# Kernel optimization log

Measured on AMD Instinct MI355X. Metric: run time of the kernel, lower is better.

Reference implementation:

```python
import math
import jax, jax.numpy as jnp
import numpy as np

# ---- module hyperparameters (from init_kwargs) ----
N_DELTA, N_THETA, N_GAMMA = 32, 64, 256
N_TOTAL = N_DELTA + N_THETA + N_GAMMA  # 352
N_DIMS = 1024
BATCH = 4096
N_STEPS = 32
DT = 0.01
COUPLING = 2.0
PAC = 0.3
EPS = 1e-6
TWO_PI = 2.0 * math.pi


def setup_inputs() -> dict:
    key = jax.random.key(0)
    k0, k1, k2 = jax.random.split(key, 3)
    x = jax.random.normal(k0, (BATCH, N_DIMS), dtype=jnp.float32)
    # xavier_uniform with gain=0.5 for Linear(n_dims, n_total, bias=False)
    bound = 0.5 * math.sqrt(6.0 / (N_DIMS + N_TOTAL))
    W_phase = jax.random.uniform(k1, (N_TOTAL, N_DIMS), jnp.float32, -bound, bound)
    W_amp = jax.random.uniform(k2, (N_TOTAL, N_DIMS), jnp.float32, -bound, bound)
    # natural angular frequencies per band: delta ~2Hz, theta ~6Hz, gamma ~40Hz
    omega = jnp.concatenate([
        jnp.full((N_DELTA,), TWO_PI * 2.0, jnp.float32),
        jnp.full((N_THETA,), TWO_PI * 6.0, jnp.float32),
        jnp.full((N_GAMMA,), TWO_PI * 40.0, jnp.float32),
    ])
    # block-diagonal intra-band Kuramoto coupling, K_ij = coupling_strength / n_band
    Kn = np.zeros((N_TOTAL, N_TOTAL), dtype=np.float32)
    o = 0
    for nb in (N_DELTA, N_THETA, N_GAMMA):
        Kn[o:o + nb, o:o + nb] = COUPLING / nb
        o += nb
    K = jnp.asarray(Kn)
    return {"x": x, "W_phase": W_phase, "W_amp": W_amp, "omega": omega, "K": K}


def reference(x, W_phase, W_amp, omega, K):
    # learned projections -> initial phase in [0, 2pi), amplitude clamped >= eps
    phase0 = (x @ W_phase.T) % TWO_PI                      # (B, n_total)
    amp0 = jnp.maximum(jnp.abs(x @ W_amp.T), EPS)          # (B, n_total)

    def step(carry, _):
        phase, amp = carry
        s, c = jnp.sin(phase), jnp.cos(phase)
        # sum_j K_ij sin(phi_j - phi_i) = cos(phi_i)*(K@sin)_i - sin(phi_i)*(K@cos)_i
        coup = c * (s @ K.T) - s * (c @ K.T)
        phase_n = (phase + DT * (omega + coup)) % TWO_PI
        d = phase_n[:, :N_DELTA]
        t = phase_n[:, N_DELTA:N_DELTA + N_THETA]
        mean_d = jnp.arctan2(jnp.sin(d).mean(-1), jnp.cos(d).mean(-1))  # (B,)
        mean_t = jnp.arctan2(jnp.sin(t).mean(-1), jnp.cos(t).mean(-1))  # (B,)
        B = phase.shape[0]
        mod = jnp.concatenate([
            jnp.zeros((B, N_DELTA), phase.dtype),
            jnp.broadcast_to((PAC * jnp.cos(mean_d))[:, None], (B, N_THETA)),
            jnp.broadcast_to((PAC * jnp.cos(mean_t))[:, None], (B, N_GAMMA)),
        ], axis=-1)
        amp_n = jnp.maximum(amp * (1.0 + DT * mod), EPS)
        return (phase_n, amp_n), None

    (final_phase, final_amp), _ = jax.lax.scan(step, (phase0, amp0), None, length=N_STEPS)
    return final_amp
```

## Files before the change

### kernel.cpp

```cpp
#include <hip/hip_runtime.h>

typedef float  f32x4 __attribute__((ext_vector_type(4)));
typedef short  s16x8 __attribute__((ext_vector_type(8)));
typedef _Float16 h2 __attribute__((ext_vector_type(2)));
typedef unsigned short u16;
typedef u16 u16x4 __attribute__((ext_vector_type(4)));

#define N_DIMS 1024
#define N_OSC  352
#define N_PH   96
#define BATCH  4096
#define EPSV   1e-6f
#define INV2PI 0.15915494309189535f

__device__ __forceinline__ u16 f2bf(float f){
  unsigned u = __builtin_bit_cast(unsigned, f);
  u += 0x7FFFu + ((u >> 16) & 1u);
  return (u16)(u >> 16);
}
__device__ __forceinline__ float bf2f(unsigned h){
  return __builtin_bit_cast(float, h << 16);
}

#define NX4 1048576
#define NWP4 24576
#define NWA4 90112
#define NCONV (NX4 + NWP4 + NWA4)

__global__ __launch_bounds__(256) void convert_k(const f32x4* __restrict__ x,
    const f32x4* __restrict__ wp, const f32x4* __restrict__ wa,
    u16x4* __restrict__ xb, u16x4* __restrict__ wb){
  int i = blockIdx.x * 256 + threadIdx.x;
  if (i >= NCONV) return;
  f32x4 v; u16x4* dst;
  if (i < NX4) { v = x[i]; dst = xb + i; }
  else {
    int j = i - NX4;
    v = (j < NWP4) ? wp[j] : wa[j - NWP4];
    dst = wb + j;
  }
  u16x4 r;
  r[0]=f2bf(v[0]); r[1]=f2bf(v[1]); r[2]=f2bf(v[2]); r[3]=f2bf(v[3]);
  *dst = r;
}

__device__ __forceinline__ void gload16(const u16* g, u16* l){
  __builtin_amdgcn_global_load_lds(
      (const __attribute__((address_space(1))) unsigned int*)(g),
      (__attribute__((address_space(3))) unsigned int*)(l), 16, 0, 0);
}

__global__ __launch_bounds__(256) void gemm_k(const u16* __restrict__ xb,
    const u16* __restrict__ wb, u16* __restrict__ phase0, float* __restrict__ amp0){
  __shared__ u16 lds[2][6144];
  const int tid = threadIdx.x;
  const int l   = tid & 63;
  const int w   = tid >> 6;

  const int bid = blockIdx.x;
  const int xcd = bid & 7;
  const int r   = bid >> 3;
  const int mt  = xcd * 8 + r / 14;
  const int nt  = r % 14;
  const int m0  = mt * 64;
  const int n0  = nt * 32;

  const int sr8  = l >> 3;
  const int scol = (((l & 7) ^ sr8) * 8);
  const u16* ga = xb + (size_t)(m0 + w*16 + sr8) * N_DIMS + scol;
  const u16* gb = wb + (size_t)(n0 + w*8  + sr8) * N_DIMS + scol;

  #define STAGE(b, kt) { \
    gload16(ga + (kt)*64,            &lds[b][w*1024]); \
    gload16(ga + (kt)*64 + 8*N_DIMS, &lds[b][w*1024 + 512]); \
    gload16(gb + (kt)*64,            &lds[b][4096 + w*512]); }

  const int rl = l & 15;
  const int q0 = l >> 4;
  const int sx = l & 7;
  const int wr = w >> 1, wc = w & 1;

  f32x4 acc[2] = {};
  STAGE(0, 0)
  __syncthreads();

  for (int kt = 0; kt < 16; kt++){
    const int cb = kt & 1;
    if (kt < 15) STAGE(cb^1, kt+1)
    s16x8 a[2][2], b[2];
    #pragma unroll
    for (int mi = 0; mi < 2; mi++)
    #pragma unroll
    for (int ks = 0; ks < 2; ks++){
      int off = (wr*32 + mi*16 + rl)*64 + (((ks*4 + q0) ^ sx) * 8);
      a[mi][ks] = *(const s16x8*)&lds[cb][off];
    }
    #pragma unroll
    for (int ks = 0; ks < 2; ks++){
      int off = 4096 + (wc*16 + rl)*64 + (((ks*4 + q0) ^ sx) * 8);
      b[ks] = *(const s16x8*)&lds[cb][off];
    }
    #pragma unroll
    for (int ks = 0; ks < 2; ks++)
    #pragma unroll
    for (int mi = 0; mi < 2; mi++)
      acc[mi] = __builtin_amdgcn_mfma_f32_16x16x32_bf16(a[mi][ks], b[ks], acc[mi], 0,0,0);
    __syncthreads();
  }
  #undef STAGE

  const int n = n0 + wc*16 + rl;
  const bool isph = (n < N_PH);
  #pragma unroll
  for (int mi = 0; mi < 2; mi++)
  #pragma unroll
  for (int rg = 0; rg < 4; rg++){
    const int m = m0 + wr*32 + mi*16 + q0*4 + rg;
    float v = acc[mi][rg];
    if (isph){ float t = v * INV2PI; t -= floorf(t); phase0[(size_t)m*N_PH + n] = f2bf(t); }
    else     { amp0[(size_t)m*N_OSC + (n - N_PH)] = fmaxf(fabsf(v), EPSV); }
  }
}

__device__ __forceinline__ int ibc(h2 v){ return __builtin_bit_cast(int, v); }
__device__ __forceinline__ h2  hbc(int v){ return __builtin_bit_cast(h2, v); }

__device__ __forceinline__ h2 rowsum16(h2 x){
  int v = ibc(x);
  v = ibc(hbc(v) + hbc(__builtin_amdgcn_mov_dpp(v, 0x121, 0xF, 0xF, true)));
  v = ibc(hbc(v) + hbc(__builtin_amdgcn_mov_dpp(v, 0x122, 0xF, 0xF, true)));
  v = ibc(hbc(v) + hbc(__builtin_amdgcn_mov_dpp(v, 0x124, 0xF, 0xF, true)));
  v = ibc(hbc(v) + hbc(__builtin_amdgcn_mov_dpp(v, 0x128, 0xF, 0xF, true)));
  return hbc(v);
}

__device__ __forceinline__ void updp(h2& s, h2& c, h2 cA, h2 sA, h2 GS, h2 GC){
  h2 e  = c*GS - s*GC;
  h2 s1 = s*cA + c*sA;
  h2 c1 = c*cA - s*sA;
  s = s1 + c1*e;
  c = c1 - s1*e;
}

__device__ __forceinline__ h2 splat2(_Float16 v){ h2 r; r[0]=v; r[1]=v; return r; }

__global__ __launch_bounds__(256) void iter_k(const u16* __restrict__ phase0,
                                              float* __restrict__ amp){
  const int tid = threadIdx.x;
  const int l   = tid & 63;
  const int g   = l & 15;
  const int row = blockIdx.x*16 + (tid>>6)*4 + (l>>4);
  const size_t rb  = (size_t)row * N_OSC;
  const size_t rbp = (size_t)row * N_PH;

  const h2 cAd = splat2((_Float16)0.99211470f), sAd = splat2((_Float16)0.12533323f);
  const h2 cAt = splat2((_Float16)0.92977649f), sAt = splat2((_Float16)0.36812455f);
  const h2 kd = splat2((_Float16)6.25e-4f);
  const h2 kt = splat2((_Float16)3.125e-4f);

  h2 sD, cD, sT[2], cT[2];
  {
    const u16* pr = phase0 + rbp;
    unsigned dw = *(const unsigned*)(pr + 2*g);
    uint2 tw    = *(const uint2*)(pr + 32 + 4*g);
    #define SC2(dS, dC, i, p0, p1) { \
      dS[i][0] = (_Float16)__builtin_amdgcn_sinf(p0); \
      dS[i][1] = (_Float16)__builtin_amdgcn_sinf(p1); \
      dC[i][0] = (_Float16)__builtin_amdgcn_cosf(p0); \
      dC[i][1] = (_Float16)__builtin_amdgcn_cosf(p1); }
    {
      float d0 = bf2f(dw & 0xFFFFu), d1 = bf2f(dw >> 16);
      sD[0] = (_Float16)__builtin_amdgcn_sinf(d0);
      sD[1] = (_Float16)__builtin_amdgcn_sinf(d1);
      cD[0] = (_Float16)__builtin_amdgcn_cosf(d0);
      cD[1] = (_Float16)__builtin_amdgcn_cosf(d1);
    }
    SC2(sT, cT, 0, bf2f(tw.x & 0xFFFFu), bf2f(tw.x >> 16))
    SC2(sT, cT, 1, bf2f(tw.y & 0xFFFFu), bf2f(tw.y >> 16))
    #undef SC2
  }

  h2 PD, PT;
  #define REDUCE { \
    h2 pd; pd[0] = sD[0]+sD[1]; pd[1] = cD[0]+cD[1]; \
    h2 ts = sT[0]+sT[1], tc = cT[0]+cT[1]; \
    h2 pt; pt[0] = ts[0]+ts[1]; pt[1] = tc[0]+tc[1]; \
    PD = rowsum16(pd); PT = rowsum16(pt); }

  REDUCE

  float Pth = 1.f, Pga = 1.f, mPth = 1.f, mPga = 1.f;
  for (int t = 0; t < 32; t++){
    h2 gd = PD * kd, gt = PT * kt;
    h2 GSd = splat2(gd[0]), GCd = splat2(gd[1]);
    h2 GSt = splat2(gt[0]), GCt = splat2(gt[1]);
    updp(sD, cD, cAd, sAd, GSd, GCd);
    updp(sT[0], cT[0], cAt, sAt, GSt, GCt);
    updp(sT[1], cT[1], cAt, sAt, GSt, GCt);
    REDUCE
    float Sd = (float)PD[0], Cd = (float)PD[1];
    float St = (float)PT[0], Ct = (float)PT[1];
    float ft = 1.f + 0.003f * Cd * __builtin_amdgcn_rsqf(Cd*Cd + Sd*Sd);
    float fg = 1.f + 0.003f * Ct * __builtin_amdgcn_rsqf(Ct*Ct + St*St);
    Pth *= ft; mPth = fminf(mPth, Pth);
    Pga *= fg; mPga = fminf(mPga, Pga);
  }
  #undef REDUCE

  const float cth = EPSV * Pth / mPth;
  const float cga = EPSV * Pga / mPga;
  {
    float4 a = *(const float4*)(amp + rb + 32 + 4*g);
    a.x = fmaxf(a.x*Pth, cth); a.y = fmaxf(a.y*Pth, cth);
    a.z = fmaxf(a.z*Pth, cth); a.w = fmaxf(a.w*Pth, cth);
    *(float4*)(amp + rb + 32 + 4*g) = a;
  }
  #pragma unroll
  for (int i = 0; i < 4; i++){
    float4 a = *(const float4*)(amp + rb + 96 + 16*g + 4*i);
    a.x = fmaxf(a.x*Pga, cga); a.y = fmaxf(a.y*Pga, cga);
    a.z = fmaxf(a.z*Pga, cga); a.w = fmaxf(a.w*Pga, cga);
    *(float4*)(amp + rb + 96 + 16*g + 4*i) = a;
  }
}

extern "C" void kernel_launch(void* const* d_in, const int* in_sizes, int n_in,
                              void* d_out, int out_size, void* d_ws, size_t ws_size,
                              hipStream_t stream){
  const float* x  = (const float*)d_in[0];
  const float* wp = (const float*)d_in[1];
  const float* wa = (const float*)d_in[2];
  float* out = (float*)d_out;
  char* ws = (char*)d_ws;
  u16* xb  = (u16*)(ws);
  u16* wb  = (u16*)(ws + 8388608);
  u16* phase0 = (u16*)(ws + 9306112);

  convert_k<<<4544, 256, 0, stream>>>((const f32x4*)x, (const f32x4*)wp, (const f32x4*)wa,
                                      (u16x4*)xb, (u16x4*)wb);
  gemm_k<<<896, 256, 0, stream>>>(xb, wb, phase0, out);
  iter_k<<<256, 256, 0, stream>>>(phase0, out);
}
```

Baseline: 31.22 us.

## Fuse phase GEMM and oscillator iteration into prep kernel, apply amp factors in GEMM epilogue

```diff
diff --git a/kernel.cpp b/kernel.cpp
--- a/kernel.cpp
+++ b/kernel.cpp
@@ -18,113 +18,27 @@
   u += 0x7FFFu + ((u >> 16) & 1u);
   return (u16)(u >> 16);
 }
-__device__ __forceinline__ float bf2f(unsigned h){
-  return __builtin_bit_cast(float, h << 16);
-}
-
-#define NX4 1048576
-#define NWP4 24576
-#define NWA4 90112
-#define NCONV (NX4 + NWP4 + NWA4)
-
-__global__ __launch_bounds__(256) void convert_k(const f32x4* __restrict__ x,
-    const f32x4* __restrict__ wp, const f32x4* __restrict__ wa,
-    u16x4* __restrict__ xb, u16x4* __restrict__ wb){
-  int i = blockIdx.x * 256 + threadIdx.x;
-  if (i >= NCONV) return;
-  f32x4 v; u16x4* dst;
-  if (i < NX4) { v = x[i]; dst = xb + i; }
-  else {
-    int j = i - NX4;
-    v = (j < NWP4) ? wp[j] : wa[j - NWP4];
-    dst = wb + j;
-  }
-  u16x4 r;
-  r[0]=f2bf(v[0]); r[1]=f2bf(v[1]); r[2]=f2bf(v[2]); r[3]=f2bf(v[3]);
-  *dst = r;
-}
-
+__device__ __forceinline__ unsigned pkbf(float a, float b){
+  unsigned r; asm("v_cvt_pk_bf16_f32 %0, %1, %2" : "=v"(r) : "v"(a), "v"(b)); return r;
+}
+__device__ __forceinline__ s16x8 mk8(f32x4 a, f32x4 b){
+  uint4 u; u.x = pkbf(a[0],a[1]); u.y = pkbf(a[2],a[3]);
+  u.z = pkbf(b[0],b[1]); u.w = pkbf(b[2],b[3]);
+  return __builtin_bit_cast(s16x8, u);
+}
 __device__ __forceinline__ void gload16(const u16* g, u16* l){
   __builtin_amdgcn_global_load_lds(
       (const __attribute__((address_space(1))) unsigned int*)(g),
       (__attribute__((address_space(3))) unsigned int*)(l), 16, 0, 0);
 }
-
-__global__ __launch_bounds__(256) void gemm_k(const u16* __restrict__ xb,
-    const u16* __restrict__ wb, u16* __restrict__ phase0, float* __restrict__ amp0){
-  __shared__ u16 lds[2][6144];
-  const int tid = threadIdx.x;
-  const int l   = tid & 63;
-  const int w   = tid >> 6;
-
-  const int bid = blockIdx.x;
-  const int xcd = bid & 7;
-  const int r   = bid >> 3;
-  const int mt  = xcd * 8 + r / 14;
-  const int nt  = r % 14;
-  const int m0  = mt * 64;
-  const int n0  = nt * 32;
-
-  const int sr8  = l >> 3;
-  const int scol = (((l & 7) ^ sr8) * 8);
-  const u16* ga = xb + (size_t)(m0 + w*16 + sr8) * N_DIMS + scol;
-  const u16* gb = wb + (size_t)(n0 + w*8  + sr8) * N_DIMS + scol;
-
-  #define STAGE(b, kt) { \
-    gload16(ga + (kt)*64,            &lds[b][w*1024]); \
-    gload16(ga + (kt)*64 + 8*N_DIMS, &lds[b][w*1024 + 512]); \
-    gload16(gb + (kt)*64,            &lds[b][4096 + w*512]); }
-
-  const int rl = l & 15;
-  const int q0 = l >> 4;
-  const int sx = l & 7;
-  const int wr = w >> 1, wc = w & 1;
-
-  f32x4 acc[2] = {};
-  STAGE(0, 0)
-  __syncthreads();
-
-  for (int kt = 0; kt < 16; kt++){
-    const int cb = kt & 1;
-    if (kt < 15) STAGE(cb^1, kt+1)
-    s16x8 a[2][2], b[2];
-    #pragma unroll
-    for (int mi = 0; mi < 2; mi++)
-    #pragma unroll
-    for (int ks = 0; ks < 2; ks++){
-      int off = (wr*32 + mi*16 + rl)*64 + (((ks*4 + q0) ^ sx) * 8);
-      a[mi][ks] = *(const s16x8*)&lds[cb][off];
-    }
-    #pragma unroll
-    for (int ks = 0; ks < 2; ks++){
-      int off = 4096 + (wc*16 + rl)*64 + (((ks*4 + q0) ^ sx) * 8);
-      b[ks] = *(const s16x8*)&lds[cb][off];
-    }
-    #pragma unroll
-    for (int ks = 0; ks < 2; ks++)
-    #pragma unroll
-    for (int mi = 0; mi < 2; mi++)
-      acc[mi] = __builtin_amdgcn_mfma_f32_16x16x32_bf16(a[mi][ks], b[ks], acc[mi], 0,0,0);
-    __syncthreads();
-  }
-  #undef STAGE
-
-  const int n = n0 + wc*16 + rl;
-  const bool isph = (n < N_PH);
-  #pragma unroll
-  for (int mi = 0; mi < 2; mi++)
-  #pragma unroll
-  for (int rg = 0; rg < 4; rg++){
-    const int m = m0 + wr*32 + mi*16 + q0*4 + rg;
-    float v = acc[mi][rg];
-    if (isph){ float t = v * INV2PI; t -= floorf(t); phase0[(size_t)m*N_PH + n] = f2bf(t); }
-    else     { amp0[(size_t)m*N_OSC + (n - N_PH)] = fmaxf(fabsf(v), EPSV); }
-  }
+__device__ __forceinline__ void gload16f(const float* g, float* l){
+  __builtin_amdgcn_global_load_lds(
+      (const __attribute__((address_space(1))) unsigned int*)(g),
+      (__attribute__((address_space(3))) unsigned int*)(l), 16, 0, 0);
 }
 
 __device__ __forceinline__ int ibc(h2 v){ return __builtin_bit_cast(int, v); }
 __device__ __forceinline__ h2  hbc(int v){ return __builtin_bit_cast(h2, v); }
-
 __device__ __forceinline__ h2 rowsum16(h2 x){
   int v = ibc(x);
   v = ibc(hbc(v) + hbc(__builtin_amdgcn_mov_dpp(v, 0x121, 0xF, 0xF, true)));
@@ -133,7 +47,6 @@
   v = ibc(hbc(v) + hbc(__builtin_amdgcn_mov_dpp(v, 0x128, 0xF, 0xF, true)));
   return hbc(v);
 }
-
 __device__ __forceinline__ void updp(h2& s, h2& c, h2 cA, h2 sA, h2 GS, h2 GC){
   h2 e  = c*GS - s*GC;
   h2 s1 = s*cA + c*sA;
@@ -141,57 +54,127 @@
   s = s1 + c1*e;
   c = c1 - s1*e;
 }
-
 __device__ __forceinline__ h2 splat2(_Float16 v){ h2 r; r[0]=v; r[1]=v; return r; }
 
-__global__ __launch_bounds__(256) void iter_k(const u16* __restrict__ phase0,
-                                              float* __restrict__ amp){
+#define NX4 1048576
+#define NWA4 90112
+
+__global__ __launch_bounds__(256) void prep_k(const float* __restrict__ x,
+    const float* __restrict__ wp, const float* __restrict__ wa,
+    u16x4* __restrict__ xb, u16x4* __restrict__ wb, float* __restrict__ factors){
+  __shared__ float ldsf[14336];
   const int tid = threadIdx.x;
-  const int l   = tid & 63;
-  const int g   = l & 15;
-  const int row = blockIdx.x*16 + (tid>>6)*4 + (l>>4);
-  const size_t rb  = (size_t)row * N_OSC;
-  const size_t rbp = (size_t)row * N_PH;
+  const int bid = blockIdx.x;
+
+  if (bid >= 256){
+    int i = (bid - 256)*256 + tid;
+    f32x4 v; u16x4* dst;
+    if (i < NX4) { v = ((const f32x4*)x)[i]; dst = xb + i; }
+    else { int j = i - NX4; v = ((const f32x4*)wa)[j]; dst = wb + j; }
+    u16x4 r;
+    r[0]=f2bf(v[0]); r[1]=f2bf(v[1]); r[2]=f2bf(v[2]); r[3]=f2bf(v[3]);
+    *dst = r;
+    return;
+  }
+
+  const int m0 = bid * 16;
+  const int l  = tid & 63;
+  const int w  = tid >> 6;
+  const int rl = l & 15;
+  const int q0 = l >> 4;
+
+  const int tr = tid >> 4;
+  const int ts = tid & 15;
+  const int ss = ts ^ tr;
+  const float* gx = x  + (size_t)(m0 + tr) * N_DIMS + ss*4;
+  const float* gw = wp + (size_t)tr * N_DIMS + ss*4;
+
+  #define PSTAGE(b, kt) { \
+    gload16f(gx + (kt)*64, &ldsf[(b)*7168 + tid*4]); \
+    _Pragma("unroll") \
+    for (int i = 0; i < 6; i++) \
+      gload16f(gw + (size_t)i*16384 + (kt)*64, &ldsf[(b)*7168 + 1024 + i*1024 + tid*4]); }
+
+  f32x4 acc[3] = {};
+  PSTAGE(0, 0)
+  __syncthreads();
+
+  const int s0 = (w & 1)*8 + q0*2;
+  const int gb = (w >> 1) * 3;
+
+  for (int kt = 0; kt < 16; kt++){
+    const int cb = kt & 1;
+    if (kt < 15) PSTAGE(cb^1, kt+1)
+    f32x4 a0 = *(const f32x4*)&ldsf[cb*7168 + rl*64 + ((s0     ^ rl) * 4)];
+    f32x4 a1 = *(const f32x4*)&ldsf[cb*7168 + rl*64 + (((s0+1) ^ rl) * 4)];
+    s16x8 af = mk8(a0, a1);
+    #pragma unroll
+    for (int ng = 0; ng < 3; ng++){
+      const int rowb = (gb + ng)*16 + rl;
+      f32x4 b0 = *(const f32x4*)&ldsf[cb*7168 + 1024 + rowb*64 + ((s0     ^ rl) * 4)];
+      f32x4 b1 = *(const f32x4*)&ldsf[cb*7168 + 1024 + rowb*64 + (((s0+1) ^ rl) * 4)];
+      acc[ng] = __builtin_amdgcn_mfma_f32_16x16x32_bf16(af, mk8(b0, b1), acc[ng], 0,0,0);
+    }
+    __syncthreads();
+  }
+  #undef PSTAGE
+
+  #pragma unroll
+  for (int ng = 0; ng < 3; ng++)
+    *(f32x4*)&ldsf[w*768 + ng*256 + l*4] = acc[ng];
+  __syncthreads();
+
+  if (!(w & 1)){
+    #pragma unroll
+    for (int ng = 0; ng < 3; ng++){
+      const int G = gb + ng;
+      f32x4 s = *(const f32x4*)&ldsf[ w   *768 + ng*256 + l*4]
+              + *(const f32x4*)&ldsf[(w+1)*768 + ng*256 + l*4];
+      #pragma unroll
+      for (int rg = 0; rg < 4; rg++){
+        const int row = q0*4 + rg;
+        float t = s[rg] * INV2PI; t -= floorf(t);
+        ldsf[4096 + row*96 + G*16 + rl] = t;
+      }
+    }
+  }
+  __syncthreads();
+
+  const int row16 = w*4 + q0;
+  const int g = rl;
+  const float* ph = &ldsf[4096 + row16*96];
 
   const h2 cAd = splat2((_Float16)0.99211470f), sAd = splat2((_Float16)0.12533323f);
   const h2 cAt = splat2((_Float16)0.92977649f), sAt = splat2((_Float16)0.36812455f);
   const h2 kd = splat2((_Float16)6.25e-4f);
-  const h2 kt = splat2((_Float16)3.125e-4f);
+  const h2 kt2 = splat2((_Float16)3.125e-4f);
 
   h2 sD, cD, sT[2], cT[2];
   {
-    const u16* pr = phase0 + rbp;
-    unsigned dw = *(const unsigned*)(pr + 2*g);
-    uint2 tw    = *(const uint2*)(pr + 32 + 4*g);
-    #define SC2(dS, dC, i, p0, p1) { \
-      dS[i][0] = (_Float16)__builtin_amdgcn_sinf(p0); \
-      dS[i][1] = (_Float16)__builtin_amdgcn_sinf(p1); \
-      dC[i][0] = (_Float16)__builtin_amdgcn_cosf(p0); \
-      dC[i][1] = (_Float16)__builtin_amdgcn_cosf(p1); }
-    {
-      float d0 = bf2f(dw & 0xFFFFu), d1 = bf2f(dw >> 16);
-      sD[0] = (_Float16)__builtin_amdgcn_sinf(d0);
-      sD[1] = (_Float16)__builtin_amdgcn_sinf(d1);
-      cD[0] = (_Float16)__builtin_amdgcn_cosf(d0);
-      cD[1] = (_Float16)__builtin_amdgcn_cosf(d1);
-    }
-    SC2(sT, cT, 0, bf2f(tw.x & 0xFFFFu), bf2f(tw.x >> 16))
-    SC2(sT, cT, 1, bf2f(tw.y & 0xFFFFu), bf2f(tw.y >> 16))
-    #undef SC2
+    float d0 = ph[2*g], d1 = ph[2*g+1];
+    float4 tw = *(const float4*)&ph[32 + 4*g];
+    sD[0] = (_Float16)__builtin_amdgcn_sinf(d0);
+    sD[1] = (_Float16)__builtin_amdgcn_sinf(d1);
+    cD[0] = (_Float16)__builtin_amdgcn_cosf(d0);
+    cD[1] = (_Float16)__builtin_amdgcn_cosf(d1);
+    sT[0][0] = (_Float16)__builtin_amdgcn_sinf(tw.x); sT[0][1] = (_Float16)__builtin_amdgcn_sinf(tw.y);
+    cT[0][0] = (_Float16)__builtin_amdgcn_cosf(tw.x); cT[0][1] = (_Float16)__builtin_amdgcn_cosf(tw.y);
+    sT[1][0] = (_Float16)__builtin_amdgcn_sinf(tw.z); sT[1][1] = (_Float16)__builtin_amdgcn_sinf(tw.w);
+    cT[1][0] = (_Float16)__builtin_amdgcn_cosf(tw.z); cT[1][1] = (_Float16)__builtin_amdgcn_cosf(tw.w);
   }
 
   h2 PD, PT;
   #define REDUCE { \
     h2 pd; pd[0] = sD[0]+sD[1]; pd[1] = cD[0]+cD[1]; \
-    h2 ts = sT[0]+sT[1], tc = cT[0]+cT[1]; \
-    h2 pt; pt[0] = ts[0]+ts[1]; pt[1] = tc[0]+tc[1]; \
+    h2 ts_ = sT[0]+sT[1], tc_ = cT[0]+cT[1]; \
+    h2 pt; pt[0] = ts_[0]+ts_[1]; pt[1] = tc_[0]+tc_[1]; \
     PD = rowsum16(pd); PT = rowsum16(pt); }
 
   REDUCE
 
   float Pth = 1.f, Pga = 1.f, mPth = 1.f, mPga = 1.f;
   for (int t = 0; t < 32; t++){
-    h2 gd = PD * kd, gt = PT * kt;
+    h2 gd = PD * kd, gt = PT * kt2;
     h2 GSd = splat2(gd[0]), GCd = splat2(gd[1]);
     h2 GSt = splat2(gt[0]), GCt = splat2(gt[1]);
     updp(sD, cD, cAd, sAd, GSd, GCd);
@@ -207,20 +190,86 @@
   }
   #undef REDUCE
 
-  const float cth = EPSV * Pth / mPth;
-  const float cga = EPSV * Pga / mPga;
-  {
-    float4 a = *(const float4*)(amp + rb + 32 + 4*g);
-    a.x = fmaxf(a.x*Pth, cth); a.y = fmaxf(a.y*Pth, cth);
-    a.z = fmaxf(a.z*Pth, cth); a.w = fmaxf(a.w*Pth, cth);
-    *(float4*)(amp + rb + 32 + 4*g) = a;
-  }
+  if (rl == 0){
+    float4 f; f.x = Pth; f.y = EPSV * Pth / mPth; f.z = Pga; f.w = EPSV * Pga / mPga;
+    *(float4*)(factors + (size_t)(m0 + row16)*4) = f;
+  }
+}
+
+__global__ __launch_bounds__(256) void gemm_k(const u16* __restrict__ xb,
+    const u16* __restrict__ wb, const float* __restrict__ factors,
+    float* __restrict__ out){
+  __shared__ u16 lds[2][6144];
+  const int tid = threadIdx.x;
+  const int l   = tid & 63;
+  const int w   = tid >> 6;
+
+  const int bid = blockIdx.x;
+  const int xcd = bid & 7;
+  const int r   = bid >> 3;
+  const int mt  = xcd * 8 + r / 11;
+  const int nt  = r % 11;
+  const int m0  = mt * 64;
+  const int n0  = nt * 32;
+
+  const int sr8  = l >> 3;
+  const int scol = (((l & 7) ^ sr8) * 8);
+  const u16* gA0 = xb + (size_t)(m0 + w*16 + sr8) * N_DIMS + scol;
+  const u16* gB0 = wb + (size_t)(n0 + w*8  + sr8) * N_DIMS + scol;
+
+  #define STAGE(b, kt) { \
+    gload16(gA0 + (kt)*64,            &lds[b][w*1024]); \
+    gload16(gA0 + (kt)*64 + 8*N_DIMS, &lds[b][w*1024 + 512]); \
+    gload16(gB0 + (kt)*64,            &lds[b][4096 + w*512]); }
+
+  const int rl = l & 15;
+  const int q0 = l >> 4;
+  const int sx = l & 7;
+  const int wr = w >> 1, wc = w & 1;
+
+  f32x4 acc[2] = {};
+  STAGE(0, 0)
+  __syncthreads();
+
+  for (int kt = 0; kt < 16; kt++){
+    const int cb = kt & 1;
+    if (kt < 15) STAGE(cb^1, kt+1)
+    s16x8 a[2][2], b[2];
+    #pragma unroll
+    for (int mi = 0; mi < 2; mi++)
+    #pragma unroll
+    for (int ks = 0; ks < 2; ks++){
+      int off = (wr*32 + mi*16 + rl)*64 + (((ks*4 + q0) ^ sx) * 8);
+      a[mi][ks] = *(const s16x8*)&lds[cb][off];
+    }
+    #pragma unroll
+    for (int ks = 0; ks < 2; ks++){
+      int off = 4096 + (wc*16 + rl)*64 + (((ks*4 + q0) ^ sx) * 8);
+      b[ks] = *(const s16x8*)&lds[cb][off];
+    }
+    #pragma unroll
+    for (int ks = 0; ks < 2; ks++)
+    #pragma unroll
+    for (int mi = 0; mi < 2; mi++)
+      acc[mi] = __builtin_amdgcn_mfma_f32_16x16x32_bf16(a[mi][ks], b[ks], acc[mi], 0,0,0);
+    __syncthreads();
+  }
+  #undef STAGE
+
+  const int n = n0 + wc*16 + rl;
+  const int cls = (nt == 0) ? 0 : ((nt < 3) ? 1 : 2);
   #pragma unroll
-  for (int i = 0; i < 4; i++){
-    float4 a = *(const float4*)(amp + rb + 96 + 16*g + 4*i);
-    a.x = fmaxf(a.x*Pga, cga); a.y = fmaxf(a.y*Pga, cga);
-    a.z = fmaxf(a.z*Pga, cga); a.w = fmaxf(a.w*Pga, cga);
-    *(float4*)(amp + rb + 96 + 16*g + 4*i) = a;
+  for (int mi = 0; mi < 2; mi++)
+  #pragma unroll
+  for (int rg = 0; rg < 4; rg++){
+    const int m = m0 + wr*32 + mi*16 + q0*4 + rg;
+    float a0 = fmaxf(fabsf(acc[mi][rg]), EPSV);
+    float o = a0;
+    if (cls != 0){
+      const float2 f = *(const float2*)(factors + (size_t)m*4 + ((cls == 2) ? 2 : 0));
+      o = fmaxf(a0 * f.x, f.y);
+    }
+    out[(size_t)m * N_OSC + n] = o;
   }
 }
 
@@ -234,10 +283,8 @@
   char* ws = (char*)d_ws;
   u16* xb  = (u16*)(ws);
   u16* wb  = (u16*)(ws + 8388608);
-  u16* phase0 = (u16*)(ws + 9306112);
-
-  convert_k<<<4544, 256, 0, stream>>>((const f32x4*)x, (const f32x4*)wp, (const f32x4*)wa,
-                                      (u16x4*)xb, (u16x4*)wb);
-  gemm_k<<<896, 256, 0, stream>>>(xb, wb, phase0, out);
-  iter_k<<<256, 256, 0, stream>>>(phase0, out);
-}
+  float* factors = (float*)(ws + 9109504);
+
+  prep_k<<<4704, 256, 0, stream>>>(x, wp, wa, (u16x4*)xb, (u16x4*)wb, factors);
+  gemm_k<<<704, 256, 0, stream>>>(xb, wb, factors, out);
+}
```

Measured after the change: 34.90 us. 1.12x slower.
